# Kernel optimization log

Hardware: AMD Instinct MI355X
Metric: run time of the kernel (lower is better)

The kernel has to match this reference:

```python
import jax, jax.numpy as jnp
import numpy as np

N_NODES = 50000
N_EDGES = 600000
IN_DIM = 128
HIDDEN = 128


def setup_inputs() -> dict:
    key = jax.random.key(0)
    k1, k2, k3, k4 = jax.random.split(key, 4)
    x = jax.random.normal(k1, (N_NODES, IN_DIM), dtype=jnp.float32)
    edge_index = jax.random.randint(k2, (2, N_EDGES), 0, N_NODES, dtype=jnp.int64)
    # Glorot-ish init for the two GCN layer weights
    W1 = jax.random.normal(k3, (IN_DIM, HIDDEN), dtype=jnp.float32) / np.sqrt(IN_DIM)
    b1 = jnp.zeros((HIDDEN,), dtype=jnp.float32)
    W2 = jax.random.normal(k4, (HIDDEN, HIDDEN), dtype=jnp.float32) / np.sqrt(HIDDEN)
    b2 = jnp.zeros((HIDDEN,), dtype=jnp.float32)
    return {"x": x, "edge_index": edge_index, "W1": W1, "b1": b1, "W2": W2, "b2": b2}


def _gcn_layer(x, W, b, src, dst, deg_inv_sqrt, n_nodes):
    # GCNConv: out = D^{-1/2} (A + I) D^{-1/2} X W + b, computed edge-wise.
    xw = x @ W                                           # [N, H] dense GEMM
    norm = deg_inv_sqrt[src] * deg_inv_sqrt[dst]         # [E+N]
    msg = xw[src] * norm[:, None]                        # gather + scale, [E+N, H]
    agg = jax.ops.segment_sum(msg, dst, num_segments=n_nodes)  # scatter-add
    return agg + b


def reference(x, edge_index, W1, b1, W2, b2):
    n_nodes = x.shape[0]
    loop = jnp.arange(n_nodes, dtype=edge_index.dtype)
    # add self-loops once; shared by both layers (same graph)
    src = jnp.concatenate([edge_index[0], loop])
    dst = jnp.concatenate([edge_index[1], loop])
    deg = jax.ops.segment_sum(jnp.ones_like(src, dtype=x.dtype), dst, num_segments=n_nodes)
    deg_inv_sqrt = jnp.where(deg > 0, jax.lax.rsqrt(jnp.maximum(deg, 1.0)), 0.0)

    h = jax.nn.relu(_gcn_layer(x, W1, b1, src, dst, deg_inv_sqrt, n_nodes))
    h = jax.nn.relu(_gcn_layer(h, W2, b2, src, dst, deg_inv_sqrt, n_nodes))
    return h
```

## Files before the change

kernel.cpp:

```cpp
#include <hip/hip_runtime.h>
#include <hip/hip_bf16.h>

#define DIM 128
#define CHUNK 4096
#define CAP 4096
typedef __hip_bfloat16 bf16;
typedef __attribute__((ext_vector_type(8))) short bf16x8;
typedef __attribute__((ext_vector_type(4))) float f32x4;

__global__ void prep_kernel(int* __restrict__ bcursor, int nbuck,
                            const int* __restrict__ ei, int E, int* __restrict__ misc,
                            const float* __restrict__ W1, const float* __restrict__ W2,
                            bf16* __restrict__ Wsw1, bf16* __restrict__ Wsw2) {
    if (blockIdx.x == 0) {
        for (int i = threadIdx.x; i < nbuck; i += 256) bcursor[i] = i * CAP;
    } else if (blockIdx.x == 1) {
        __shared__ int s_or;
        if (threadIdx.x == 0) s_or = 0;
        __syncthreads();
        int lim = E < 16384 ? E : 16384;
        int acc = 0;
        for (int j = threadIdx.x; j < lim; j += 256) acc |= ei[2 * j + 1];
        if (acc) atomicOr(&s_or, 1);
        __syncthreads();
        if (threadIdx.x == 0) misc[1] = s_or;
    } else {
        int id = (blockIdx.x - 2) * 256 + threadIdx.x;
        const float* W = (id < 2048) ? W1 : W2;
        bf16* Wsw = (id < 2048) ? Wsw1 : Wsw2;
        int t = id & 2047;
        int f = t >> 6, l = t & 63;
        int kt = f >> 3, nt = f & 7;
        int q = l >> 4, m = l & 15;
        bf16 tmp[8];
        #pragma unroll
        for (int j = 0; j < 8; ++j)
            tmp[j] = __float2bfloat16(W[(size_t)(kt * 32 + q * 8 + j) * DIM + nt * 16 + m]);
        *(bf16x8*)(Wsw + (size_t)t * 8) = *(const bf16x8*)tmp;
    }
}

__device__ __forceinline__ void gemm_body(const float* __restrict__ Xv,
                                          const bf16* __restrict__ Wsw,
                                          bf16* __restrict__ Y, int N,
                                          int gw, int nw, int lane,
                                          float* sld) {
    int m = lane & 15, q = lane >> 4;
    const bf16x8* bp = (const bf16x8*)Wsw;
    bf16x8 wreg[32];
    #pragma unroll
    for (int f = 0; f < 32; ++f) wreg[f] = bp[(size_t)f * 64 + lane];
    for (int t = gw; t * 16 + 16 <= N; t += nw) {
        int base = t * 16;
        bf16x8 a[4];
        const float* xp = Xv + (size_t)(base + m) * DIM + q * 8;
        #pragma unroll
        for (int kt = 0; kt < 4; ++kt) {
            float4 v0 = *(const float4*)(xp + kt * 32);
            float4 v1 = *(const float4*)(xp + kt * 32 + 4);
            bf16 tt[8] = {__float2bfloat16(v0.x), __float2bfloat16(v0.y),
                          __float2bfloat16(v0.z), __float2bfloat16(v0.w),
                          __float2bfloat16(v1.x), __float2bfloat16(v1.y),
                          __float2bfloat16(v1.z), __float2bfloat16(v1.w)};
            a[kt] = *(const bf16x8*)tt;
        }
        f32x4 acc[8];
        #pragma unroll
        for (int nt = 0; nt < 8; ++nt) acc[nt] = (f32x4){0.f, 0.f, 0.f, 0.f};
        #pragma unroll
        for (int kt = 0; kt < 4; ++kt) {
            #pragma unroll
            for (int nt = 0; nt < 8; ++nt)
                acc[nt] = __builtin_amdgcn_mfma_f32_16x16x32_bf16(a[kt], wreg[kt * 8 + nt],
                                                                  acc[nt], 0, 0, 0);
        }
        #pragma unroll
        for (int nt = 0; nt < 8; ++nt)
            #pragma unroll
            for (int r = 0; r < 4; ++r)
                sld[(q * 4 + r) * 132 + nt * 16 + m] = acc[nt][r];
        asm volatile("s_waitcnt lgkmcnt(0)" ::: "memory");
        #pragma unroll
        for (int i = 0; i < 4; ++i) {
            int row = i * 4 + q;
            const float* rp = sld + row * 132 + m * 8;
            float4 v0 = *(const float4*)rp;
            float4 v1 = *(const float4*)(rp + 4);
            alignas(16) bf16 tt[8] = {
                __float2bfloat16(v0.x), __float2bfloat16(v0.y),
                __float2bfloat16(v0.z), __float2bfloat16(v0.w),
                __float2bfloat16(v1.x), __float2bfloat16(v1.y),
                __float2bfloat16(v1.z), __float2bfloat16(v1.w)};
            *(uint4*)(Y + (size_t)(base + row) * DIM + m * 8) = *(const uint4*)tt;
        }
        asm volatile("s_waitcnt lgkmcnt(0)" ::: "memory");
    }
}

__global__ __launch_bounds__(256)
void scatter_gemm1(const int* __restrict__ ei, int E, const int* __restrict__ misc,
                   int* __restrict__ bcursor, unsigned* __restrict__ staged,
                   int nbuck, int nchunks,
                   const float* __restrict__ X, const bf16* __restrict__ Wsw,
                   bf16* __restrict__ Y, int N) {
    __shared__ float smem[4][16 * 132];
    int bx = blockIdx.x;
    if (bx < nchunks) {
        int* s_cnt  = (int*)&smem[0][0];
        int* s_base = s_cnt + 512;
        int* s_fill = s_cnt + 1024;
        for (int i = threadIdx.x; i < nbuck; i += 256) { s_cnt[i] = 0; s_fill[i] = 0; }
        __syncthreads();
        int flagI = misc[1];
        int c0 = bx * CHUNK;
        int cn = min(E - c0, CHUNK);
        for (int i = threadIdx.x; i < cn; i += 256) {
            int e = c0 + i;
            int d = (flagI == 0) ? ei[2 * E + 2 * e] : ei[E + e];
            atomicAdd(&s_cnt[d >> 7], 1);
        }
        __syncthreads();
        for (int i = threadIdx.x; i < nbuck; i += 256) {
            int c = s_cnt[i];
            s_base[i] = c ? atomicAdd(&bcursor[i], c) : 0;
        }
        __syncthreads();
        for (int i = threadIdx.x; i < cn; i += 256) {
            int e = c0 + i;
            int s, d;
            if (flagI == 0) { s = ei[2 * e]; d = ei[2 * E + 2 * e]; }
            else            { s = ei[e];     d = ei[E + e]; }
            int b = d >> 7;
            int r = s_base[b] + atomicAdd(&s_fill[b], 1);
            if (r < (b + 1) * CAP)
                staged[r] = ((unsigned)s << 7) | (unsigned)(d & 127);
        }
    } else {
        int wid = threadIdx.x >> 6, lane = threadIdx.x & 63;
        int ngw = (gridDim.x - nchunks) * 4;
        gemm_body(X, Wsw, Y, N, (bx - nchunks) * 4 + wid, ngw, lane, smem[wid]);
    }
}

__global__ void bucket_sort(const unsigned* __restrict__ staged,
                            const int* __restrict__ bcursor,
                            int* __restrict__ csr, int* __restrict__ rowstart,
                            int* __restrict__ cnt, float* __restrict__ dis, int N) {
    __shared__ int s_cnt[128], s_off[128], s_fill[128], s_scan[128];
    int b = blockIdx.x, tid = threadIdx.x;
    int seg0 = b * CAP;
    int n = min(bcursor[b] - seg0, CAP);
    if (tid < 128) { s_cnt[tid] = 0; s_fill[tid] = 0; }
    __syncthreads();
    for (int i = tid; i < n; i += 256)
        atomicAdd(&s_cnt[staged[seg0 + i] & 127u], 1);
    __syncthreads();
    int v = (tid < 128) ? s_cnt[tid] : 0;
    if (tid < 128) s_scan[tid] = v;
    __syncthreads();
    for (int off = 1; off < 128; off <<= 1) {
        int t = (tid < 128 && tid >= off) ? s_scan[tid - off] : 0;
        __syncthreads();
        if (tid < 128) s_scan[tid] += t;
        __syncthreads();
    }
    if (tid < 128) {
        s_off[tid] = s_scan[tid] - v;
        int node = b * 128 + tid;
        if (node < N) {
            cnt[node] = v;
            rowstart[node] = seg0 + s_off[tid];
            dis[node] = rsqrtf((float)(v + 1));
        }
    }
    __syncthreads();
    for (int i = tid; i < n; i += 256) {
        unsigned p = staged[seg0 + i];
        int dl = p & 127u;
        int r = atomicAdd(&s_fill[dl], 1);
        csr[seg0 + s_off[dl] + r] = (int)(p >> 7);
    }
}

__device__ __forceinline__ void fma8(float* a, uint4 v, float ds) {
    a[0] = fmaf(__uint_as_float(v.x << 16), ds, a[0]);
    a[1] = fmaf(__uint_as_float(v.x & 0xffff0000u), ds, a[1]);
    a[2] = fmaf(__uint_as_float(v.y << 16), ds, a[2]);
    a[3] = fmaf(__uint_as_float(v.y & 0xffff0000u), ds, a[3]);
    a[4] = fmaf(__uint_as_float(v.z << 16), ds, a[4]);
    a[5] = fmaf(__uint_as_float(v.z & 0xffff0000u), ds, a[5]);
    a[6] = fmaf(__uint_as_float(v.w << 16), ds, a[6]);
    a[7] = fmaf(__uint_as_float(v.w & 0xffff0000u), ds, a[7]);
}

__device__ __forceinline__ void add8(float* a, uint4 v) {
    a[0] += __uint_as_float(v.x << 16);
    a[1] += __uint_as_float(v.x & 0xffff0000u);
    a[2] += __uint_as_float(v.y << 16);
    a[3] += __uint_as_float(v.y & 0xffff0000u);
    a[4] += __uint_as_float(v.z << 16);
    a[5] += __uint_as_float(v.z & 0xffff0000u);
    a[6] += __uint_as_float(v.w << 16);
    a[7] += __uint_as_float(v.w & 0xffff0000u);
}

__global__ __launch_bounds__(256, 4)
void agg1_gemm2(const uint4* __restrict__ Y, const int* __restrict__ rowstart,
                const int* __restrict__ cnt, const int* __restrict__ csr,
                const float* __restrict__ dis, const float* __restrict__ bias,
                const bf16* __restrict__ Wsw, bf16* __restrict__ Y2, int N) {
    __shared__ __align__(16) bf16 h_lds[16][136];
    __shared__ float s_out[16 * 132];
    int wave = threadIdx.x >> 6, lane = threadIdx.x & 63;
    int sub = lane >> 4, cl = lane & 15;
    int base = blockIdx.x * 16;
    int node = base + wave * 4 + sub;
    bool alive = node < N;

    float acc[4][8];
    #pragma unroll
    for (int j = 0; j < 4; ++j)
        #pragma unroll
        for (int k = 0; k < 8; ++k) acc[j][k] = 0.f;

    float dn = 0.f;
    if (alive) {
        int e0 = rowstart[node], e1 = e0 + cnt[node];
        dn = dis[node];
        fma8(acc[3], Y[(size_t)node * 16 + cl], dn);

        int e = e0;
        while (e + 8 <= e1) {
            int s[8];
            #pragma unroll
            for (int j = 0; j < 8; ++j) s[j] = csr[e + j];
            uint4 v[8]; float dv[8];
            #pragma unroll
            for (int j = 0; j < 8; ++j) { v[j] = Y[(size_t)s[j] * 16 + cl]; dv[j] = dis[s[j]]; }
            #pragma unroll
            for (int j = 0; j < 8; ++j) fma8(acc[j & 3], v[j], dv[j]);
            e += 8;
        }
        if (e + 4 <= e1) {
            int s[4];
            #pragma unroll
            for (int j = 0; j < 4; ++j) s[j] = csr[e + j];
            uint4 v[4]; float dv[4];
            #pragma unroll
            for (int j = 0; j < 4; ++j) { v[j] = Y[(size_t)s[j] * 16 + cl]; dv[j] = dis[s[j]]; }
            #pragma unroll
            for (int j = 0; j < 4; ++j) fma8(acc[j], v[j], dv[j]);
            e += 4;
        }
        for (; e < e1; ++e) {
            int s = csr[e];
            fma8(acc[0], Y[(size_t)s * 16 + cl], dis[s]);
        }
    }
    {
        float s8[8];
        #pragma unroll
        for (int k = 0; k < 8; ++k)
            s8[k] = (acc[0][k] + acc[1][k]) + (acc[2][k] + acc[3][k]);
        float4 b0 = ((const float4*)bias)[2 * cl];
        float4 b1 = ((const float4*)bias)[2 * cl + 1];
        alignas(16) bf16 t[8];
        t[0] = __float2bfloat16(alive ? fmaxf(dn * s8[0] + b0.x, 0.f) : 0.f);
        t[1] = __float2bfloat16(alive ? fmaxf(dn * s8[1] + b0.y, 0.f) : 0.f);
        t[2] = __float2bfloat16(alive ? fmaxf(dn * s8[2] + b0.z, 0.f) : 0.f);
        t[3] = __float2bfloat16(alive ? fmaxf(dn * s8[3] + b0.w, 0.f) : 0.f);
        t[4] = __float2bfloat16(alive ? fmaxf(dn * s8[4] + b1.x, 0.f) : 0.f);
        t[5] = __float2bfloat16(alive ? fmaxf(dn * s8[5] + b1.y, 0.f) : 0.f);
        t[6] = __float2bfloat16(alive ? fmaxf(dn * s8[6] + b1.z, 0.f) : 0.f);
        t[7] = __float2bfloat16(alive ? fmaxf(dn * s8[7] + b1.w, 0.f) : 0.f);
        *(uint4*)&h_lds[wave * 4 + sub][cl * 8] = *(const uint4*)t;
    }
    __syncthreads();

    int m = cl, q = sub;
    bf16x8 a[4];
    #pragma unroll
    for (int kt = 0; kt < 4; ++kt)
        a[kt] = *(const bf16x8*)&h_lds[m][q * 8 + kt * 32];
    const bf16x8* bp = (const bf16x8*)Wsw;
    f32x4 g[2];
    g[0] = (f32x4){0.f, 0.f, 0.f, 0.f};
    g[1] = (f32x4){0.f, 0.f, 0.f, 0.f};
    #pragma unroll
    for (int kt = 0; kt < 4; ++kt) {
        #pragma unroll
        for (int j = 0; j < 2; ++j) {
            int nt = wave * 2 + j;
            bf16x8 bfr = bp[(size_t)(kt * 8 + nt) * 64 + lane];
            g[j] = __builtin_amdgcn_mfma_f32_16x16x32_bf16(a[kt], bfr, g[j], 0, 0, 0);
        }
    }
    #pragma unroll
    for (int j = 0; j < 2; ++j)
        #pragma unroll
        for (int r = 0; r < 4; ++r)
            s_out[(q * 4 + r) * 132 + (wave * 2 + j) * 16 + m] = g[j][r];
    __syncthreads();

    int on = threadIdx.x >> 4;
    int oc = (threadIdx.x & 15) * 8;
    if (base + on < N) {
        float ds = dis[base + on];
        const float* rp = s_out + on * 132 + oc;
        float4 v0 = *(const float4*)rp;
        float4 v1 = *(const float4*)(rp + 4);
        alignas(16) bf16 t[8] = {
            __float2bfloat16(v0.x * ds), __float2bfloat16(v0.y * ds),
            __float2bfloat16(v0.z * ds), __float2bfloat16(v0.w * ds),
            __float2bfloat16(v1.x * ds), __float2bfloat16(v1.y * ds),
            __float2bfloat16(v1.z * ds), __float2bfloat16(v1.w * ds)};
        *(uint4*)(Y2 + (size_t)(base + on) * DIM + oc) = *(const uint4*)t;
    }
}

__global__ __launch_bounds__(256, 4)
void aggregate_final(const uint4* __restrict__ Y, const int* __restrict__ rowstart,
                     const int* __restrict__ cnt, const int* __restrict__ csr,
                     const float* __restrict__ dis, const float* __restrict__ bias,
                     float* __restrict__ Of, int N) {
    int wave = threadIdx.x >> 6;
    int lane = threadIdx.x & 63;
    int sub = lane >> 4, cl = lane & 15;
    int node = blockIdx.x * 16 + wave * 4 + sub;
    if (node >= N) return;
    int e0 = rowstart[node], e1 = e0 + cnt[node];

    float acc[4][8];
    #pragma unroll
    for (int j = 0; j < 4; ++j)
        #pragma unroll
        for (int k = 0; k < 8; ++k) acc[j][k] = 0.f;

    float dn = dis[node];
    add8(acc[3], Y[(size_t)node * 16 + cl]);

    int e = e0;
    while (e + 12 <= e1) {
        int s[12];
        #pragma unroll
        for (int j = 0; j < 12; ++j) s[j] = csr[e + j];
        uint4 v[12];
        #pragma unroll
        for (int j = 0; j < 12; ++j) v[j] = Y[(size_t)s[j] * 16 + cl];
        #pragma unroll
        for (int j = 0; j < 12; ++j) add8(acc[j & 3], v[j]);
        e += 12;
    }
    if (e + 8 <= e1) {
        int s[8];
        #pragma unroll
        for (int j = 0; j < 8; ++j) s[j] = csr[e + j];
        uint4 v[8];
        #pragma unroll
        for (int j = 0; j < 8; ++j) v[j] = Y[(size_t)s[j] * 16 + cl];
        #pragma unroll
        for (int j = 0; j < 8; ++j) add8(acc[j & 3], v[j]);
        e += 8;
    }
    if (e + 4 <= e1) {
        int s[4];
        #pragma unroll
        for (int j = 0; j < 4; ++j) s[j] = csr[e + j];
        uint4 v[4];
        #pragma unroll
        for (int j = 0; j < 4; ++j) v[j] = Y[(size_t)s[j] * 16 + cl];
        #pragma unroll
        for (int j = 0; j < 4; ++j) add8(acc[j], v[j]);
        e += 4;
    }
    for (; e < e1; ++e)
        add8(acc[0], Y[(size_t)csr[e] * 16 + cl]);

    float s8[8];
    #pragma unroll
    for (int k = 0; k < 8; ++k)
        s8[k] = (acc[0][k] + acc[1][k]) + (acc[2][k] + acc[3][k]);

    float4 b0 = ((const float4*)bias)[2 * cl];
    float4 b1 = ((const float4*)bias)[2 * cl + 1];
    f32x4 o0, o1;
    o0[0] = fmaxf(dn * s8[0] + b0.x, 0.f);
    o0[1] = fmaxf(dn * s8[1] + b0.y, 0.f);
    o0[2] = fmaxf(dn * s8[2] + b0.z, 0.f);
    o0[3] = fmaxf(dn * s8[3] + b0.w, 0.f);
    o1[0] = fmaxf(dn * s8[4] + b1.x, 0.f);
    o1[1] = fmaxf(dn * s8[5] + b1.y, 0.f);
    o1[2] = fmaxf(dn * s8[6] + b1.z, 0.f);
    o1[3] = fmaxf(dn * s8[7] + b1.w, 0.f);
    f32x4* op = (f32x4*)(Of + (size_t)node * DIM + cl * 8);
    __builtin_nontemporal_store(o0, op);
    __builtin_nontemporal_store(o1, op + 1);
}

extern "C" void kernel_launch(void* const* d_in, const int* in_sizes, int n_in,
                              void* d_out, int out_size, void* d_ws, size_t ws_size,
                              hipStream_t stream) {
    const float* x  = (const float*)d_in[0];
    const int*   ei = (const int*)d_in[1];
    const float* W1 = (const float*)d_in[2];
    const float* b1 = (const float*)d_in[3];
    const float* W2 = (const float*)d_in[4];
    const float* b2 = (const float*)d_in[5];

    int N = in_sizes[0] / DIM;
    int E = in_sizes[1] / 2;
    int nbuck = (N + 127) / 128;
    int nchunks = (E + CHUNK - 1) / CHUNK;

    char* w = (char*)d_ws;
    size_t used = 0;
    auto carve = [&](size_t bytes) {
        char* p = w + used;
        used += (bytes + 255) & ~(size_t)255;
        return p;
    };
    int*      misc     = (int*)     carve(256);
    int*      bcursor  = (int*)     carve((size_t)(nbuck + 1) * 4);
    unsigned* staged   = (unsigned*)carve((size_t)nbuck * CAP * 4);
    int*      csr      = (int*)     carve((size_t)nbuck * CAP * 4);
    int*      rowstart = (int*)     carve((size_t)N * 4);
    int*      cnt      = (int*)     carve((size_t)N * 4);
    float*    dis      = (float*)   carve((size_t)N * 4);
    bf16*     ybuf     = (bf16*)    carve((size_t)N * DIM * 2);
    bf16*     hbuf     = (bf16*)    carve((size_t)N * DIM * 2);
    bf16*     Wsw1     = (bf16*)    carve((size_t)DIM * DIM * 2);
    bf16*     Wsw2     = (bf16*)    carve((size_t)DIM * DIM * 2);

    prep_kernel <<<18, 256, 0, stream>>>(bcursor, nbuck, ei, E, misc, W1, W2, Wsw1, Wsw2);
    scatter_gemm1<<<nchunks + 196, 256, 0, stream>>>(ei, E, misc, bcursor, staged,
                                                     nbuck, nchunks, x, Wsw1, ybuf, N);
    bucket_sort <<<nbuck, 256, 0, stream>>>(staged, bcursor, csr, rowstart, cnt, dis, N);

    int ablocks = (N + 15) / 16;
    agg1_gemm2<<<ablocks, 256, 0, stream>>>((const uint4*)ybuf, rowstart, cnt, csr,
                                            dis, b1, Wsw2, hbuf, N);
    aggregate_final<<<ablocks, 256, 0, stream>>>((const uint4*)hbuf, rowstart, cnt, csr,
                                                 dis, b2, (float*)d_out, N);
}
```

Before: 179.8 us.

## Fuse bucket sort into scatter/GEMM kernel with a global completion counter

Folds the bucket_sort pass into the scatter+GEMM1 launch as extra blocks. Those blocks spin on a global atomic counter that each scatter block increments after a threadfence, so sorting can overlap with the GEMM blocks and one kernel launch disappears. This relies on the scatter blocks being scheduled before the spinning sort blocks; block indices put them first, but that ordering is not guaranteed. The spinning blocks also hold CUs while they wait.

```diff
diff --git a/kernel.cpp b/kernel.cpp
--- a/kernel.cpp
+++ b/kernel.cpp
@@ -14,6 +14,7 @@
                             bf16* __restrict__ Wsw1, bf16* __restrict__ Wsw2) {
     if (blockIdx.x == 0) {
         for (int i = threadIdx.x; i < nbuck; i += 256) bcursor[i] = i * CAP;
+        if (threadIdx.x == 0) misc[2] = 0;
     } else if (blockIdx.x == 1) {
         __shared__ int s_or;
         if (threadIdx.x == 0) s_or = 0;
@@ -98,34 +99,37 @@
 }
 
 __global__ __launch_bounds__(256)
-void scatter_gemm1(const int* __restrict__ ei, int E, const int* __restrict__ misc,
-                   int* __restrict__ bcursor, unsigned* __restrict__ staged,
-                   int nbuck, int nchunks,
-                   const float* __restrict__ X, const bf16* __restrict__ Wsw,
-                   bf16* __restrict__ Y, int N) {
+void scatter_gemm1_sort(const int* __restrict__ ei, int E, int* __restrict__ misc,
+                        int* __restrict__ bcursor, unsigned* __restrict__ staged,
+                        int nbuck, int nchunks, int ngemm,
+                        const float* __restrict__ X, const bf16* __restrict__ Wsw,
+                        bf16* __restrict__ Y,
+                        int* __restrict__ csr, int* __restrict__ rowstart,
+                        int* __restrict__ cnt, float* __restrict__ dis, int N) {
     __shared__ float smem[4][16 * 132];
     int bx = blockIdx.x;
+    int tid = threadIdx.x;
     if (bx < nchunks) {
         int* s_cnt  = (int*)&smem[0][0];
         int* s_base = s_cnt + 512;
         int* s_fill = s_cnt + 1024;
-        for (int i = threadIdx.x; i < nbuck; i += 256) { s_cnt[i] = 0; s_fill[i] = 0; }
+        for (int i = tid; i < nbuck; i += 256) { s_cnt[i] = 0; s_fill[i] = 0; }
         __syncthreads();
         int flagI = misc[1];
         int c0 = bx * CHUNK;
         int cn = min(E - c0, CHUNK);
-        for (int i = threadIdx.x; i < cn; i += 256) {
+        for (int i = tid; i < cn; i += 256) {
             int e = c0 + i;
             int d = (flagI == 0) ? ei[2 * E + 2 * e] : ei[E + e];
             atomicAdd(&s_cnt[d >> 7], 1);
         }
         __syncthreads();
-        for (int i = threadIdx.x; i < nbuck; i += 256) {
+        for (int i = tid; i < nbuck; i += 256) {
             int c = s_cnt[i];
             s_base[i] = c ? atomicAdd(&bcursor[i], c) : 0;
         }
         __syncthreads();
-        for (int i = threadIdx.x; i < cn; i += 256) {
+        for (int i = tid; i < cn; i += 256) {
             int e = c0 + i;
             int s, d;
             if (flagI == 0) { s = ei[2 * e]; d = ei[2 * E + 2 * e]; }
@@ -135,50 +139,57 @@
             if (r < (b + 1) * CAP)
                 staged[r] = ((unsigned)s << 7) | (unsigned)(d & 127);
         }
+        __syncthreads();
+        __threadfence();
+        if (tid == 0) atomicAdd(&misc[2], 1);
+    } else if (bx < nchunks + ngemm) {
+        int wid = tid >> 6, lane = tid & 63;
+        int ngw = ngemm * 4;
+        gemm_body(X, Wsw, Y, N, (bx - nchunks - 0) * 4 + wid, ngw, lane, smem[wid]);
     } else {
-        int wid = threadIdx.x >> 6, lane = threadIdx.x & 63;
-        int ngw = (gridDim.x - nchunks) * 4;
-        gemm_body(X, Wsw, Y, N, (bx - nchunks) * 4 + wid, ngw, lane, smem[wid]);
-    }
-}
-
-__global__ void bucket_sort(const unsigned* __restrict__ staged,
-                            const int* __restrict__ bcursor,
-                            int* __restrict__ csr, int* __restrict__ rowstart,
-                            int* __restrict__ cnt, float* __restrict__ dis, int N) {
-    __shared__ int s_cnt[128], s_off[128], s_fill[128], s_scan[128];
-    int b = blockIdx.x, tid = threadIdx.x;
-    int seg0 = b * CAP;
-    int n = min(bcursor[b] - seg0, CAP);
-    if (tid < 128) { s_cnt[tid] = 0; s_fill[tid] = 0; }
-    __syncthreads();
-    for (int i = tid; i < n; i += 256)
-        atomicAdd(&s_cnt[staged[seg0 + i] & 127u], 1);
-    __syncthreads();
-    int v = (tid < 128) ? s_cnt[tid] : 0;
-    if (tid < 128) s_scan[tid] = v;
-    __syncthreads();
-    for (int off = 1; off < 128; off <<= 1) {
-        int t = (tid < 128 && tid >= off) ? s_scan[tid - off] : 0;
-        __syncthreads();
-        if (tid < 128) s_scan[tid] += t;
-        __syncthreads();
-    }
-    if (tid < 128) {
-        s_off[tid] = s_scan[tid] - v;
-        int node = b * 128 + tid;
-        if (node < N) {
-            cnt[node] = v;
-            rowstart[node] = seg0 + s_off[tid];
-            dis[node] = rsqrtf((float)(v + 1));
-        }
-    }
-    __syncthreads();
-    for (int i = tid; i < n; i += 256) {
-        unsigned p = staged[seg0 + i];
-        int dl = p & 127u;
-        int r = atomicAdd(&s_fill[dl], 1);
-        csr[seg0 + s_off[dl] + r] = (int)(p >> 7);
+        if (tid == 0) {
+            while (__hip_atomic_load(&misc[2], __ATOMIC_ACQUIRE,
+                                     __HIP_MEMORY_SCOPE_AGENT) < nchunks)
+                __builtin_amdgcn_s_sleep(8);
+        }
+        __syncthreads();
+        int* s_cnt  = (int*)&smem[0][0];
+        int* s_off  = s_cnt + 128;
+        int* s_fill = s_cnt + 256;
+        int* s_scan = s_cnt + 384;
+        int b = bx - nchunks - ngemm;
+        int seg0 = b * CAP;
+        int n = min(bcursor[b] - seg0, CAP);
+        if (tid < 128) { s_cnt[tid] = 0; s_fill[tid] = 0; }
+        __syncthreads();
+        for (int i = tid; i < n; i += 256)
+            atomicAdd(&s_cnt[staged[seg0 + i] & 127u], 1);
+        __syncthreads();
+        int v = (tid < 128) ? s_cnt[tid] : 0;
+        if (tid < 128) s_scan[tid] = v;
+        __syncthreads();
+        for (int off = 1; off < 128; off <<= 1) {
+            int t = (tid < 128 && tid >= off) ? s_scan[tid - off] : 0;
+            __syncthreads();
+            if (tid < 128) s_scan[tid] += t;
+            __syncthreads();
+        }
+        if (tid < 128) {
+            s_off[tid] = s_scan[tid] - v;
+            int node = b * 128 + tid;
+            if (node < N) {
+                cnt[node] = v;
+                rowstart[node] = seg0 + s_off[tid];
+                dis[node] = rsqrtf((float)(v + 1));
+            }
+        }
+        __syncthreads();
+        for (int i = tid; i < n; i += 256) {
+            unsigned p = staged[seg0 + i];
+            int dl = p & 127u;
+            int r = atomicAdd(&s_fill[dl], 1);
+            csr[seg0 + s_off[dl] + r] = (int)(p >> 7);
+        }
     }
 }
 
@@ -411,6 +422,7 @@
     int E = in_sizes[1] / 2;
     int nbuck = (N + 127) / 128;
     int nchunks = (E + CHUNK - 1) / CHUNK;
+    int ngemm = 196;
 
     char* w = (char*)d_ws;
     size_t used = 0;
@@ -432,9 +444,9 @@
     bf16*     Wsw2     = (bf16*)    carve((size_t)DIM * DIM * 2);
 
     prep_kernel <<<18, 256, 0, stream>>>(bcursor, nbuck, ei, E, misc, W1, W2, Wsw1, Wsw2);
-    scatter_gemm1<<<nchunks + 196, 256, 0, stream>>>(ei, E, misc, bcursor, staged,
-                                                     nbuck, nchunks, x, Wsw1, ybuf, N);
-    bucket_sort <<<nbuck, 256, 0, stream>>>(staged, bcursor, csr, rowstart, cnt, dis, N);
+    scatter_gemm1_sort<<<nchunks + ngemm + nbuck, 256, 0, stream>>>(
+        ei, E, misc, bcursor, staged, nbuck, nchunks, ngemm,
+        x, Wsw1, ybuf, csr, rowstart, cnt, dis, N);
 
     int ablocks = (N + 15) / 16;
     agg1_gemm2<<<ablocks, 256, 0, stream>>>((const uint4*)ybuf, rowstart, cnt, csr,
```

After: 316.5 us. +76.1%, slower.
